# Optimization experiments

Measured on AMD Instinct MI355X. Metric: run time of the kernel, lower is better.

The kernel has to match this reference:

```python
import jax, jax.numpy as jnp
import numpy as np

H = 9
N1, N2, N3 = 100000, 25000, 6250
E1, E2, E3 = 1200000, 300000, 75000
LAYERS = {"l1": (6, 32), "l2": (32, 64), "l3": (64, 128), "l4": (128, 128),
          "r1": (128, 64), "r2": (128, 64), "r3": (64, 32), "r4": (64, 32)}


def setup_inputs() -> dict:
    key = jax.random.key(0)
    ks = iter(jax.random.split(key, 64))
    d = {}
    d["x"] = jax.random.normal(next(ks), (N1, 6), jnp.float32)
    d["ei1"] = jax.random.randint(next(ks), (2, E1), 0, N1)
    d["ei2"] = jax.random.randint(next(ks), (2, E2), 0, N2)
    d["ei3"] = jax.random.randint(next(ks), (2, E3), 0, N3)
    d["clust2"] = jax.random.randint(next(ks), (N1,), 0, N2)
    d["clust3"] = jax.random.randint(next(ks), (N2,), 0, N3)
    for name, (cin, cout) in LAYERS.items():
        d[name + "_u"] = jax.random.normal(next(ks), (cin, H), jnp.float32) * 0.1
        d[name + "_c"] = jax.random.normal(next(ks), (H,), jnp.float32) * 0.1
        d[name + "_w"] = jax.random.normal(next(ks), (cin, H * cout), jnp.float32) * (1.0 / np.sqrt(cin))
        d[name + "_b"] = jnp.zeros((cout,), jnp.float32)
    d["fc1_w"] = jax.random.normal(next(ks), (32, 1024), jnp.float32) * (1.0 / np.sqrt(32))
    d["fc1_b"] = jnp.zeros((1024,), jnp.float32)
    d["fc2_w"] = jax.random.normal(next(ks), (1024, 3), jnp.float32) * (1.0 / np.sqrt(1024))
    d["fc2_b"] = jnp.zeros((3,), jnp.float32)
    return d


def _feast(x, ei, u, c, W, b):
    """FeaStConv (Verma et al., PyG semantics): per-edge head attention
    q = softmax(u^T (x_j - x_i) + c), mean aggregation, self-loops added."""
    n = x.shape[0]
    out = W.shape[1] // H
    loop = jnp.arange(n)
    src = jnp.concatenate([ei[0], loop])  # message source j
    dst = jnp.concatenate([ei[1], loop])  # message target i
    q = jax.nn.softmax((x[src] - x[dst]) @ u + c, axis=1)  # [E, H]
    msg = jnp.zeros((src.shape[0], out), x.dtype)
    for h in range(H):  # fixed head loop keeps peak memory at [E, out]
        msg = msg + q[:, h:h + 1] * (x @ W[:, h * out:(h + 1) * out])[src]
    agg = jax.ops.segment_sum(msg, dst, num_segments=n)
    cnt = jax.ops.segment_sum(jnp.ones((dst.shape[0],), x.dtype), dst, num_segments=n)
    return agg / cnt[:, None] + b  # cnt >= 1 thanks to self-loops


def _pool_mean(x, clust, n_out):
    s = jax.ops.segment_sum(x, clust, num_segments=n_out)
    c = jax.ops.segment_sum(jnp.ones((x.shape[0],), x.dtype), clust, num_segments=n_out)
    return s / jnp.maximum(c, 1.0)[:, None]


def _lrelu(v):
    return jax.nn.leaky_relu(v, 0.1)


def reference(x, ei1, ei2, ei3, clust2, clust3,
              l1_u, l1_c, l1_w, l1_b, l2_u, l2_c, l2_w, l2_b,
              l3_u, l3_c, l3_w, l3_b, l4_u, l4_c, l4_w, l4_b,
              r1_u, r1_c, r1_w, r1_b, r2_u, r2_c, r2_w, r2_b,
              r3_u, r3_c, r3_w, r3_b, r4_u, r4_c, r4_w, r4_b,
              fc1_w, fc1_b, fc2_w, fc2_b):
    x1 = _lrelu(_feast(x, ei1, l1_u, l1_c, l1_w, l1_b))           # [N1, 32]
    x2 = _pool_mean(x1, clust2, N2)                                # [N2, 32]
    x2 = _lrelu(_feast(x2, ei2, l2_u, l2_c, l2_w, l2_b))           # [N2, 64]
    x3 = _pool_mean(x2, clust3, N3)                                # [N3, 64]
    x3 = _lrelu(_feast(x3, ei3, l3_u, l3_c, l3_w, l3_b))           # [N3, 128]
    x3 = _lrelu(_feast(x3, ei3, l4_u, l4_c, l4_w, l4_b))           # [N3, 128]
    f2 = _feast(x3[clust3], ei2, r1_u, r1_c, r1_w, r1_b)           # unpool -> [N2, 64] (no act)
    x2 = jnp.concatenate([x2, f2], axis=1)                         # [N2, 128]
    x2 = _lrelu(_feast(x2, ei2, r2_u, r2_c, r2_w, r2_b))           # [N2, 64]
    f1 = _feast(x2[clust2], ei1, r3_u, r3_c, r3_w, r3_b)           # unpool -> [N1, 32] (no act)
    x1 = jnp.concatenate([x1, f1], axis=1)                         # [N1, 64]
    y = _lrelu(_feast(x1, ei1, r4_u, r4_c, r4_w, r4_b))            # [N1, 32]
    y = _lrelu(y @ fc1_w + fc1_b)                                  # [N1, 1024]
    y = y @ fc2_w + fc2_b                                          # [N1, 3]
    return y / jnp.maximum(jnp.linalg.norm(y, axis=1, keepdims=True), 1e-12)
```

## Files before the change

### kernel.cpp

```cpp
#include <hip/hip_runtime.h>
#include <cstddef>
#include <cstdint>

#define NH 9
#define QLD 16

typedef _Float16 f16x8 __attribute__((ext_vector_type(8)));
typedef _Float16 f16x4 __attribute__((ext_vector_type(4)));
typedef _Float16 f16x2 __attribute__((ext_vector_type(2)));
typedef float f32x4 __attribute__((ext_vector_type(4)));

static const int cN1 = 100000, cN2 = 25000, cN3 = 6250;
static const int cE1 = 1200000, cE2 = 300000, cE3 = 75000;

static inline unsigned ceil_div(size_t a, size_t b) { return (unsigned)((a + b - 1) / b); }

struct PackArgs {
    const float* W[8];
    const float* c[8];
    const float* u[8];
    int K[8], OUT[8], Kpad[8], base[8];
    int total;
};

__global__ void pack_b_all(PackArgs a, _Float16* __restrict__ wt)
{
    int i = blockIdx.x * 256 + threadIdx.x;
    if (i >= a.total) return;
    int li = 0;
#pragma unroll
    for (int j = 1; j < 8; ++j) li += (i >= a.base[j]);
    int r = i - a.base[li];
    int Kp = a.Kpad[li], K = a.K[li], OUT = a.OUT[li];
    int NC = NH * OUT, NCO = NC + OUT;
    int n = r / Kp, k = r % Kp;
    float v = 0.f;
    if (k < K) {
        if (n < NC) v = a.W[li][(size_t)k * NC + n];
        else if (n < NCO) {
            const float* cv = a.c[li];
            float t[NH], m = -1e30f;
#pragma unroll
            for (int h = 0; h < NH; ++h) { t[h] = cv[h]; m = fmaxf(m, t[h]); }
            float den = 0.f;
#pragma unroll
            for (int h = 0; h < NH; ++h) { t[h] = __expf(t[h] - m); den += t[h]; }
            int o = n - NC;
            float acc = 0.f;
#pragma unroll
            for (int h = 0; h < NH; ++h) acc += t[h] * a.W[li][(size_t)k * NC + h * OUT + o];
            v = acc / den;
        } else {
            v = a.u[li][(size_t)k * NH + (n - NCO)];
        }
    }
    wt[i] = (_Float16)v;
}

template <typename AT>
__global__ __launch_bounds__(256) void gemm_merged(
    const AT* __restrict__ A, int lda, const int* __restrict__ ridx,
    const _Float16* __restrict__ WT, int kpad,
    _Float16* __restrict__ C, _Float16* __restrict__ xuh,
    int M, int K, int NC, int OUT)
{
    const int N = NC + OUT + NH;
    const int NCO = NC + OUT;
    const int ldc = NCO + 16;
    const int BM = 64, BK = 32, LK = 40;
    __shared__ _Float16 As[BM][LK];
    __shared__ _Float16 Bs[64][LK];
    const int tid = threadIdx.x;
    const int row0 = blockIdx.y * BM, col0 = blockIdx.x * 64;
    const int lane = tid & 63, wv = tid >> 6;
    const int g = lane >> 4, r16 = lane & 15;
    const int wr = wv >> 1, wc = wv & 1;
    f32x4 acc[2][2] = {};
    for (int k0 = 0; k0 < K; k0 += BK) {
        if constexpr (sizeof(AT) == 2) {
            int r = tid >> 2, c0 = (tid & 3) * 8;
            int gr = row0 + r, gk = k0 + c0;
            f16x8 h = {};
            if (gr < M) {
                int ar = ridx ? ridx[gr] : gr;
                h = *(const f16x8*)((const _Float16*)A + (size_t)ar * lda + gk);
            }
            *(f16x8*)&As[r][c0] = h;
        } else {
            for (int l = tid; l < 512; l += 256) {
                int r = l >> 3, c0 = (l & 7) * 4;
                int gr = row0 + r, gk = k0 + c0;
                float v0 = 0.f, v1 = 0.f, v2 = 0.f, v3 = 0.f;
                if (gr < M) {
                    int ar = ridx ? ridx[gr] : gr;
                    const float* ap = (const float*)A + (size_t)ar * lda + gk;
                    if (gk < K)     v0 = ap[0];
                    if (gk + 1 < K) v1 = ap[1];
                    if (gk + 2 < K) v2 = ap[2];
                    if (gk + 3 < K) v3 = ap[3];
                }
                f16x4 h;
                h[0] = (_Float16)v0; h[1] = (_Float16)v1; h[2] = (_Float16)v2; h[3] = (_Float16)v3;
                *(f16x4*)&As[r][c0] = h;
            }
        }
        {
            int nn = tid >> 2, c0 = (tid & 3) * 8;
            int gn = col0 + nn, gk = k0 + c0;
            f16x8 h = {};
            if (gn < N) h = *(const f16x8*)(WT + (size_t)gn * kpad + gk);
            *(f16x8*)&Bs[nn][c0] = h;
        }
        __syncthreads();
        f16x8 af[2], bf[2];
#pragma unroll
        for (int i = 0; i < 2; ++i) af[i] = *(const f16x8*)&As[wr * 32 + i * 16 + r16][g * 8];
#pragma unroll
        for (int j = 0; j < 2; ++j) bf[j] = *(const f16x8*)&Bs[wc * 32 + j * 16 + r16][g * 8];
#pragma unroll
        for (int i = 0; i < 2; ++i)
#pragma unroll
            for (int j = 0; j < 2; ++j)
                acc[i][j] = __builtin_amdgcn_mfma_f32_16x16x32_f16(af[i], bf[j], acc[i][j], 0, 0, 0);
        __syncthreads();
    }
#pragma unroll
    for (int i = 0; i < 2; ++i)
#pragma unroll
        for (int j = 0; j < 2; ++j) {
            int gc = col0 + wc * 32 + j * 16 + r16;
            if (gc >= N) continue;
            int tcol = gc - NCO;
#pragma unroll
            for (int rr = 0; rr < 4; ++rr) {
                int gr = row0 + wr * 32 + i * 16 + g * 4 + rr;
                if (gr >= M) continue;
                _Float16 val = (_Float16)acc[i][j][rr];
                C[(size_t)gr * ldc + gc] = val;
                if (tcol >= 0) xuh[(size_t)gr * QLD + tcol] = val;
            }
        }
}

__global__ void count_idx(const int* __restrict__ idx, int n, int* __restrict__ cnt)
{
    int i = blockIdx.x * 256 + threadIdx.x;
    if (i < n) atomicAdd(&cnt[idx[i]], 1);
}

__global__ void count_both(const int* __restrict__ src, const int* __restrict__ dst, int E,
                           int* __restrict__ scnt, int* __restrict__ dcnt)
{
    int i = blockIdx.x * 256 + threadIdx.x;
    if (i >= E) return;
    atomicAdd(&scnt[src[i]], 1);
    atomicAdd(&dcnt[dst[i]], 1);
}

__global__ __launch_bounds__(1024) void scan1(const int* __restrict__ in, int* __restrict__ out,
                                              int* __restrict__ part, int n)
{
    __shared__ int wsum[16];
    const int tid = threadIdx.x, lane = tid & 63, wv = tid >> 6;
    int i = blockIdx.x * 1024 + tid;
    int v = (i < n) ? in[i] : 0;
    int acc = v;
#pragma unroll
    for (int off = 1; off < 64; off <<= 1) {
        int t = __shfl_up(acc, off);
        if (lane >= off) acc += t;
    }
    if (lane == 63) wsum[wv] = acc;
    __syncthreads();
    if (wv == 0 && lane < 16) {
        int s = wsum[lane];
        int a2 = s;
#pragma unroll
        for (int off = 1; off < 16; off <<= 1) {
            int t = __shfl_up(a2, off);
            if (lane >= off) a2 += t;
        }
        wsum[lane] = a2 - s;
    }
    __syncthreads();
    int ex = wsum[wv] + acc - v;
    if (i < n) out[i] = ex;
    if (part && tid == 1023) part[blockIdx.x] = ex + v;
}

__global__ void scan_add(int* __restrict__ out, const int* __restrict__ part, int n)
{
    int i = blockIdx.x * 1024 + threadIdx.x;
    if (i < n) out[i] += part[blockIdx.x];
}

__global__ void fill_src(const int* __restrict__ soffB, const int* __restrict__ scnt,
                         int* __restrict__ srcs, int n, int ebias)
{
    int i = blockIdx.x * 256 + threadIdx.x;
    if (i >= n) return;
    int b = soffB[i] - ebias, c = scnt[i];
    for (int k = 0; k < c; ++k) srcs[b + k] = i;
}

__global__ void scatter_light(const int* __restrict__ src, const int* __restrict__ dst, int E,
                              const int* __restrict__ soffB, int* __restrict__ curs,
                              const int* __restrict__ doff, int* __restrict__ curd,
                              int2* __restrict__ erec, int ebias)
{
    int e = blockIdx.x * 256 + threadIdx.x;
    if (e >= E) return;
    int s = src[e], d = dst[e];
    int ps = soffB[s] - ebias + atomicAdd(&curs[s], 1);
    int pd = doff[d] + atomicAdd(&curd[d], 1);
    erec[ps] = make_int2(d, pd);
}

template <int OUT>
__global__ __launch_bounds__(256) void feast_msg(
    const int* __restrict__ srcs, const int2* __restrict__ erec, int E,
    const _Float16* __restrict__ xwa, const _Float16* __restrict__ xuh,
    const float* __restrict__ cvec, _Float16* __restrict__ msg)
{
    constexpr int NC = NH * OUT, NCO = NC + OUT, LDR = NCO + 16;
    const int T = OUT / 16;
    size_t tid = (size_t)blockIdx.x * 256 + threadIdx.x;
    int e = (int)(tid / T);
    int ch = (int)(tid % T);
    if (e >= E) return;
    int s = srcs[e];
    int2 ed = erec[e];
    int d = ed.x, pd = ed.y;
    f16x8 u8s = *(const f16x8*)(xwa + (size_t)s * LDR + NCO);
    f16x2 u2s = *(const f16x2*)(xwa + (size_t)s * LDR + NCO + 8);
    f16x8 u8d = *(const f16x8*)(xuh + (size_t)d * QLD);
    f16x2 u2d = *(const f16x2*)(xuh + (size_t)d * QLD + 8);
    float t[NH];
    float m = -1e30f;
#pragma unroll
    for (int h = 0; h < 8; ++h) {
        t[h] = (float)u8s[h] - (float)u8d[h] + cvec[h];
        m = fmaxf(m, t[h]);
    }
    t[8] = (float)u2s[0] - (float)u2d[0] + cvec[8];
    m = fmaxf(m, t[8]);
    float den = 0.f;
#pragma unroll
    for (int h = 0; h < NH; ++h) { t[h] = __expf(t[h] - m); den += t[h]; }
    float sc = 1.f / den;

    const f16x8* xrow = (const f16x8*)(xwa + (size_t)s * LDR) + ch * 2;
    float acc[16] = {};
#pragma unroll
    for (int h = 0; h < NH; ++h) {
        float qh = t[h] * sc;
        f16x8 a = xrow[h * (OUT / 8)];
        f16x8 b = xrow[h * (OUT / 8) + 1];
#pragma unroll
        for (int j = 0; j < 8; ++j) {
            acc[j]     += qh * (float)a[j];
            acc[8 + j] += qh * (float)b[j];
        }
    }
    f16x8* mo = (f16x8*)(msg + (size_t)pd * OUT + ch * 16);
    f16x8 r0, r1;
#pragma unroll
    for (int j = 0; j < 8; ++j) {
        r0[j] = (_Float16)acc[j];
        r1[j] = (_Float16)acc[8 + j];
    }
    mo[0] = r0;
    mo[1] = r1;
}

template <int OUT>
__global__ __launch_bounds__(256) void feast_red(
    const int* __restrict__ ds,
    const _Float16* __restrict__ msg, const _Float16* __restrict__ xwa,
    const float* __restrict__ bias, _Float16* __restrict__ outp,
    int n, int ldo, int col0, int act,
    const int* __restrict__ clust, float* __restrict__ pooled)
{
    constexpr int NC = NH * OUT, LDR = NC + OUT + 16;
    const int L = OUT / 8;
    size_t tid = (size_t)blockIdx.x * 256 + threadIdx.x;
    int d = (int)(tid / L);
    int p = (int)(tid % L);
    if (d >= n) return;
    int beg = ds[d];
    int end = ds[d + 1];
    int deg = end - beg;
    float acc[8] = {};
    int i = beg;
    for (; i + 4 <= end; i += 4) {
        f16x8 v0 = *(const f16x8*)(msg + (size_t)i * OUT + p * 8);
        f16x8 v1 = *(const f16x8*)(msg + (size_t)(i + 1) * OUT + p * 8);
        f16x8 v2 = *(const f16x8*)(msg + (size_t)(i + 2) * OUT + p * 8);
        f16x8 v3 = *(const f16x8*)(msg + (size_t)(i + 3) * OUT + p * 8);
#pragma unroll
        for (int j = 0; j < 8; ++j)
            acc[j] += ((float)v0[j] + (float)v1[j]) + ((float)v2[j] + (float)v3[j]);
    }
    for (; i < end; ++i) {
        f16x8 v0 = *(const f16x8*)(msg + (size_t)i * OUT + p * 8);
#pragma unroll
        for (int j = 0; j < 8; ++j) acc[j] += (float)v0[j];
    }
    float sc = 1.f / (float)(deg + 1);
    f16x8 sv = *(const f16x8*)(xwa + (size_t)d * LDR + NC + p * 8);
    float o[8];
    f16x8 oh;
#pragma unroll
    for (int j = 0; j < 8; ++j) {
        float v = (acc[j] + (float)sv[j]) * sc + bias[p * 8 + j];
        if (act) v = v > 0.f ? v : 0.1f * v;
        o[j] = v;
        oh[j] = (_Float16)v;
    }
    *(f16x8*)(outp + (size_t)d * ldo + col0 + p * 8) = oh;
    if (clust) {
        float* pp = pooled + (size_t)clust[d] * OUT + p * 8;
#pragma unroll
        for (int j = 0; j < 8; ++j) unsafeAtomicAdd(&pp[j], o[j]);
    }
}

__global__ void pool_div(float* __restrict__ pooled, const int* __restrict__ pcnt, int C, int m)
{
    size_t tid = (size_t)blockIdx.x * 256 + threadIdx.x;
    int j = (int)(tid / C);
    if (j >= m) return;
    pooled[tid] /= fmaxf((float)pcnt[j], 1.f);
}

__global__ void w1_to_f16t(const float* __restrict__ w1, _Float16* __restrict__ w1t)
{
    int i = blockIdx.x * 256 + threadIdx.x;
    if (i >= 32 * 1024) return;
    int n = i >> 5, k = i & 31;
    w1t[i] = (_Float16)w1[k * 1024 + n];
}

__global__ __launch_bounds__(256) void fc_head2(
    const _Float16* __restrict__ yin, const _Float16* __restrict__ w1t,
    const float* __restrict__ b1, const float* __restrict__ w2,
    const float* __restrict__ b2, float* __restrict__ outp, int n)
{
    const int lane = threadIdx.x & 63, wv = threadIdx.x >> 6;
    const int g = lane >> 4, r16 = lane & 15;
    const int node0 = blockIdx.x * 64 + wv * 16;

    f16x8 afrag = {};
    int anode = node0 + r16;
    if (anode < n) afrag = *(const f16x8*)(yin + (size_t)anode * 32 + g * 8);

    float o0[4] = {0.f, 0.f, 0.f, 0.f};
    float o1[4] = {0.f, 0.f, 0.f, 0.f};
    float o2[4] = {0.f, 0.f, 0.f, 0.f};
    const f32x4 zero4 = {0.f, 0.f, 0.f, 0.f};

#pragma unroll 2
    for (int t = 0; t < 64; ++t) {
        const f16x8 bfrag = *(const f16x8*)(w1t + ((size_t)(t * 16 + r16)) * 32 + g * 8);
        f32x4 d = __builtin_amdgcn_mfma_f32_16x16x32_f16(afrag, bfrag, zero4, 0, 0, 0);
        int kh = t * 16 + r16;
        float b1v = b1[kh];
        float w20 = w2[kh * 3], w21 = w2[kh * 3 + 1], w22 = w2[kh * 3 + 2];
#pragma unroll
        for (int r = 0; r < 4; ++r) {
            float h = d[r] + b1v;
            h = h > 0.f ? h : 0.1f * h;
            o0[r] += h * w20;
            o1[r] += h * w21;
            o2[r] += h * w22;
        }
    }
#pragma unroll
    for (int r = 0; r < 4; ++r) {
#pragma unroll
        for (int off = 1; off < 16; off <<= 1) {
            o0[r] += __shfl_xor(o0[r], off);
            o1[r] += __shfl_xor(o1[r], off);
            o2[r] += __shfl_xor(o2[r], off);
        }
    }
    if (r16 == 0) {
#pragma unroll
        for (int r = 0; r < 4; ++r) {
            int node = node0 + g * 4 + r;
            if (node >= n) continue;
            float v0 = o0[r] + b2[0];
            float v1 = o1[r] + b2[1];
            float v2 = o2[r] + b2[2];
            float nr = fmaxf(sqrtf(v0 * v0 + v1 * v1 + v2 * v2), 1e-12f);
            outp[(size_t)node * 3 + 0] = v0 / nr;
            outp[(size_t)node * 3 + 1] = v1 / nr;
            outp[(size_t)node * 3 + 2] = v2 / nr;
        }
    }
}

static void launch_msg(int outC, const int* srcs, const int2* erec, int E,
                       const _Float16* xwa, const _Float16* xuh, const float* cvec,
                       _Float16* msg, hipStream_t stream)
{
    dim3 g(ceil_div((size_t)E * (outC / 16), 256));
    if (outC == 32)       feast_msg<32><<<g, 256, 0, stream>>>(srcs, erec, E, xwa, xuh, cvec, msg);
    else if (outC == 64)  feast_msg<64><<<g, 256, 0, stream>>>(srcs, erec, E, xwa, xuh, cvec, msg);
    else                  feast_msg<128><<<g, 256, 0, stream>>>(srcs, erec, E, xwa, xuh, cvec, msg);
}

static void launch_red(int outC, const int* ds,
                       const _Float16* msg, const _Float16* xwa, const float* bias,
                       _Float16* outp, int n, int ldo, int col0, int act,
                       const int* clust, float* pooled, hipStream_t stream)
{
    dim3 g(ceil_div((size_t)n * (outC / 8), 256));
    if (outC == 32)       feast_red<32><<<g, 256, 0, stream>>>(ds, msg, xwa, bias, outp, n, ldo, col0, act, clust, pooled);
    else if (outC == 64)  feast_red<64><<<g, 256, 0, stream>>>(ds, msg, xwa, bias, outp, n, ldo, col0, act, clust, pooled);
    else                  feast_red<128><<<g, 256, 0, stream>>>(ds, msg, xwa, bias, outp, n, ldo, col0, act, clust, pooled);
}

extern "C" void kernel_launch(void* const* d_in, const int* in_sizes, int n_in,
                              void* d_out, int out_size, void* d_ws, size_t ws_size,
                              hipStream_t stream)
{
    const float* x      = (const float*)d_in[0];
    const int*   ei1    = (const int*)d_in[1];
    const int*   ei2    = (const int*)d_in[2];
    const int*   ei3    = (const int*)d_in[3];
    const int*   clust2 = (const int*)d_in[4];
    const int*   clust3 = (const int*)d_in[5];
    const float* lp[8][4];
    for (int i = 0; i < 8; ++i)
        for (int j = 0; j < 4; ++j)
            lp[i][j] = (const float*)d_in[6 + i * 4 + j];
    const float* fc1_w = (const float*)d_in[38];
    const float* fc1_b = (const float*)d_in[39];
    const float* fc2_w = (const float*)d_in[40];
    const float* fc2_b = (const float*)d_in[41];
    float* out = (float*)d_out;

    static const int lK[8]   = {6, 32, 64, 128, 128, 128, 64, 64};
    static const int lOUT[8] = {32, 64, 128, 128, 64, 64, 32, 32};

    char* ws = (char*)d_ws;
    size_t off = 0;
    auto alloc = [&](size_t b) { size_t p = off; off += (b + 255) & ~(size_t)255; return p; };
    _Float16* XWA = (_Float16*)(ws + alloc((size_t)cN1 * 336 * 2));
    _Float16* MSG = (_Float16*)(ws + alloc((size_t)cE1 * 32 * 2));
    _Float16* XUH = (_Float16*)(ws + alloc((size_t)cN1 * QLD * 2));
    _Float16* X1CAT = (_Float16*)(ws + alloc((size_t)cN1 * 64 * 2));
    _Float16* X2CAT = (_Float16*)(ws + alloc((size_t)cN2 * 128 * 2));
    _Float16* X2B   = (_Float16*)(ws + alloc((size_t)cN2 * 64 * 2));
    _Float16* X3    = (_Float16*)(ws + alloc((size_t)cN3 * 128 * 2));
    _Float16* YB    = (_Float16*)(ws + alloc((size_t)cN1 * 32 * 2));
    float* GATH = (float*)(ws + alloc((size_t)cN2 * 32 * 4));
    float* P3   = (float*)(ws + alloc((size_t)cN3 * 64 * 4));
    int* SRCS1 = (int*)(ws + alloc((size_t)cE1 * 4));
    int* SRCS2 = (int*)(ws + alloc((size_t)cE2 * 4));
    int* SRCS3 = (int*)(ws + alloc((size_t)cE3 * 4));
    int2* EREC1 = (int2*)(ws + alloc((size_t)cE1 * 8));
    int2* EREC2 = (int2*)(ws + alloc((size_t)cE2 * 8));
    int2* EREC3 = (int2*)(ws + alloc((size_t)cE3 * 8));
    int* DS1 = (int*)(ws + alloc((size_t)2 * cN1 * 4));
    int* DS2 = (int*)(ws + alloc((size_t)2 * cN2 * 4));
    int* DS3 = (int*)(ws + alloc((size_t)2 * cN3 * 4));
    size_t zn = (size_t)4 * (cN1 + cN2 + cN3) + cN2 + cN3;
    int* ZBLK = (int*)(ws + alloc(zn * 4));
    int* CB1 = ZBLK;
    int* CURS1 = CB1 + 2 * cN1;
    int* CURD1 = CURS1 + cN1;
    int* CB2 = CURD1 + cN1;
    int* CURS2 = CB2 + 2 * cN2;
    int* CURD2 = CURS2 + cN2;
    int* CB3 = CURD2 + cN2;
    int* CURS3 = CB3 + 2 * cN3;
    int* CURD3 = CURS3 + cN3;
    int* PC2 = CURD3 + cN3;
    int* PC3 = PC2 + cN2;
    int* PART = (int*)(ws + alloc(1024 * 4));
    _Float16* W1T = (_Float16*)(ws + alloc((size_t)32 * 1024 * 2));
    PackArgs pa;
    int ptot = 0;
    for (int i = 0; i < 8; ++i) {
        pa.W[i] = lp[i][2]; pa.c[i] = lp[i][1]; pa.u[i] = lp[i][0];
        pa.K[i] = lK[i]; pa.OUT[i] = lOUT[i];
        pa.Kpad[i] = (lK[i] + 31) & ~31;
        pa.base[i] = ptot;
        ptot += (NH * lOUT[i] + lOUT[i] + NH) * pa.Kpad[i];
    }
    pa.total = ptot;
    _Float16* WT = (_Float16*)(ws + alloc((size_t)ptot * 2));

    auto run_scan = [&](const int* in, int* outp, int n) {
        int nb = (n + 1023) / 1024;
        scan1<<<nb, 1024, 0, stream>>>(in, outp, nb > 1 ? PART : nullptr, n);
        if (nb > 1) {
            scan1<<<1, 1024, 0, stream>>>(PART, PART, nullptr, nb);
            scan_add<<<nb, 1024, 0, stream>>>(outp, PART, n);
        }
    };

    hipMemsetAsync(ZBLK, 0, zn * 4, stream);

    auto build = [&](const int* ei, int E, int n, int* cb, int* curs, int* curd, int* ds,
                     int* srcs, int2* erec) {
        count_both<<<ceil_div(E, 256), 256, 0, stream>>>(ei, ei + E, E, cb + n, cb);
        run_scan(cb, ds, 2 * n);
        fill_src<<<ceil_div(n, 256), 256, 0, stream>>>(ds + n, cb + n, srcs, n, E);
        scatter_light<<<ceil_div(E, 256), 256, 0, stream>>>(ei, ei + E, E, ds + n, curs, ds, curd, erec, E);
    };
    build(ei1, cE1, cN1, CB1, CURS1, CURD1, DS1, SRCS1, EREC1);
    build(ei2, cE2, cN2, CB2, CURS2, CURD2, DS2, SRCS2, EREC2);
    build(ei3, cE3, cN3, CB3, CURS3, CURD3, DS3, SRCS3, EREC3);

    pack_b_all<<<ceil_div(ptot, 256), 256, 0, stream>>>(pa, WT);
    w1_to_f16t<<<ceil_div(32 * 1024, 256), 256, 0, stream>>>(fc1_w, W1T);

    auto feast = [&](auto* xin, int ldx, const int* ridx, int n, int cin, int li,
                     const int* srcs, const int2* erec, const int* ds, int E,
                     _Float16* dstp, int ldo, int col0, int act,
                     const int* pclust, float* pooled) {
        int outC = lOUT[li];
        int NC = NH * outC;
        int N = NC + outC + NH;
        gemm_merged<<<dim3(ceil_div(N, 64), ceil_div(n, 64)), 256, 0, stream>>>(
            xin, ldx, ridx, WT + (size_t)pa.base[li], pa.Kpad[li], XWA, XUH, n, cin, NC, outC);
        launch_msg(outC, srcs, erec, E, XWA, XUH, lp[li][1], MSG, stream);
        launch_red(outC, ds, MSG, XWA, lp[li][3], dstp, n, ldo, col0, act, pclust, pooled, stream);
    };

    hipMemsetAsync(GATH, 0, (size_t)cN2 * 32 * 4, stream);
    count_idx<<<ceil_div(cN1, 256), 256, 0, stream>>>(clust2, cN1, PC2);
    feast(x, 6, nullptr, cN1, 6, 0, SRCS1, EREC1, DS1, cE1, X1CAT, 64, 0, 1, clust2, GATH);
    pool_div<<<ceil_div((size_t)cN2 * 32, 256), 256, 0, stream>>>(GATH, PC2, 32, cN2);

    count_idx<<<ceil_div(cN2, 256), 256, 0, stream>>>(clust3, cN2, PC3);
    hipMemsetAsync(P3, 0, (size_t)cN3 * 64 * 4, stream);
    feast(GATH, 32, nullptr, cN2, 32, 1, SRCS2, EREC2, DS2, cE2, X2CAT, 128, 0, 1, clust3, P3);
    pool_div<<<ceil_div((size_t)cN3 * 64, 256), 256, 0, stream>>>(P3, PC3, 64, cN3);

    feast(P3, 64, nullptr, cN3, 64, 2, SRCS3, EREC3, DS3, cE3, X3, 128, 0, 1, nullptr, nullptr);
    feast(X3, 128, nullptr, cN3, 128, 3, SRCS3, EREC3, DS3, cE3, X3, 128, 0, 1, nullptr, nullptr);

    feast(X3, 128, clust3, cN2, 128, 4, SRCS2, EREC2, DS2, cE2, X2CAT, 128, 64, 0, nullptr, nullptr);

    feast(X2CAT, 128, nullptr, cN2, 128, 5, SRCS2, EREC2, DS2, cE2, X2B, 64, 0, 1, nullptr, nullptr);

    feast(X2B, 64, clust2, cN1, 64, 6, SRCS1, EREC1, DS1, cE1, X1CAT, 64, 32, 0, nullptr, nullptr);

    feast(X1CAT, 64, nullptr, cN1, 64, 7, SRCS1, EREC1, DS1, cE1, YB, 32, 0, 1, nullptr, nullptr);

    fc_head2<<<ceil_div(cN1, 64), 256, 0, stream>>>(YB, W1T, fc1_b, fc2_w, fc2_b, out, cN1);

    (void)in_sizes; (void)n_in; (void)out_size; (void)ws_size;
}
```

Before: 991.3 us.

## Two-pass coarse binning of edges by source before CSR scatter

```diff
diff --git a/kernel.cpp b/kernel.cpp
--- a/kernel.cpp
+++ b/kernel.cpp
@@ -148,13 +148,16 @@
     if (i < n) atomicAdd(&cnt[idx[i]], 1);
 }
 
-__global__ void count_both(const int* __restrict__ src, const int* __restrict__ dst, int E,
-                           int* __restrict__ scnt, int* __restrict__ dcnt)
+__global__ void count_b3(const int* __restrict__ src, const int* __restrict__ dst, int E,
+                         int* __restrict__ scnt, int* __restrict__ dcnt,
+                         int* __restrict__ bcnt, int shift)
 {
     int i = blockIdx.x * 256 + threadIdx.x;
     if (i >= E) return;
-    atomicAdd(&scnt[src[i]], 1);
+    int s = src[i];
+    atomicAdd(&scnt[s], 1);
     atomicAdd(&dcnt[dst[i]], 1);
+    atomicAdd(&bcnt[s >> shift], 1);
 }
 
 __global__ __launch_bounds__(1024) void scan1(const int* __restrict__ in, int* __restrict__ out,
@@ -203,14 +206,27 @@
     for (int k = 0; k < c; ++k) srcs[b + k] = i;
 }
 
-__global__ void scatter_light(const int* __restrict__ src, const int* __restrict__ dst, int E,
-                              const int* __restrict__ soffB, int* __restrict__ curs,
-                              const int* __restrict__ doff, int* __restrict__ curd,
-                              int2* __restrict__ erec, int ebias)
+__global__ void bin_pass1(const int* __restrict__ src, const int* __restrict__ dst, int E,
+                          const int* __restrict__ boff, int* __restrict__ bcur,
+                          int2* __restrict__ tmp, int shift)
 {
     int e = blockIdx.x * 256 + threadIdx.x;
     if (e >= E) return;
-    int s = src[e], d = dst[e];
+    int s = src[e];
+    int b = s >> shift;
+    int p = boff[b] + atomicAdd(&bcur[b], 1);
+    tmp[p] = make_int2(s, dst[e]);
+}
+
+__global__ void bin_pass2(const int2* __restrict__ tmp, int E,
+                          const int* __restrict__ soffB, int* __restrict__ curs,
+                          const int* __restrict__ doff, int* __restrict__ curd,
+                          int2* __restrict__ erec, int ebias)
+{
+    int e = blockIdx.x * 256 + threadIdx.x;
+    if (e >= E) return;
+    int2 rec = tmp[e];
+    int s = rec.x, d = rec.y;
     int ps = soffB[s] - ebias + atomicAdd(&curs[s], 1);
     int pd = doff[d] + atomicAdd(&curd[d], 1);
     erec[ps] = make_int2(d, pd);
@@ -443,6 +459,10 @@
 
     static const int lK[8]   = {6, 32, 64, 128, 128, 128, 64, 64};
     static const int lOUT[8] = {32, 64, 128, 128, 64, 64, 32, 32};
+    static const int lSH[3]  = {5, 3, 1};
+    const int NB1 = ceil_div(cN1, 1 << lSH[0]);
+    const int NB2 = ceil_div(cN2, 1 << lSH[1]);
+    const int NB3 = ceil_div(cN3, 1 << lSH[2]);
 
     char* ws = (char*)d_ws;
     size_t off = 0;
@@ -463,21 +483,29 @@
     int2* EREC1 = (int2*)(ws + alloc((size_t)cE1 * 8));
     int2* EREC2 = (int2*)(ws + alloc((size_t)cE2 * 8));
     int2* EREC3 = (int2*)(ws + alloc((size_t)cE3 * 8));
+    int2* TMP = (int2*)(ws + alloc((size_t)cE1 * 8));
     int* DS1 = (int*)(ws + alloc((size_t)2 * cN1 * 4));
     int* DS2 = (int*)(ws + alloc((size_t)2 * cN2 * 4));
     int* DS3 = (int*)(ws + alloc((size_t)2 * cN3 * 4));
-    size_t zn = (size_t)4 * (cN1 + cN2 + cN3) + cN2 + cN3;
+    int* BOFF = (int*)(ws + alloc((size_t)4096 * 4));
+    size_t zn = (size_t)4 * (cN1 + cN2 + cN3) + 2 * (NB1 + NB2 + NB3) + cN2 + cN3;
     int* ZBLK = (int*)(ws + alloc(zn * 4));
     int* CB1 = ZBLK;
     int* CURS1 = CB1 + 2 * cN1;
     int* CURD1 = CURS1 + cN1;
-    int* CB2 = CURD1 + cN1;
+    int* BCNT1 = CURD1 + cN1;
+    int* BCUR1 = BCNT1 + NB1;
+    int* CB2 = BCUR1 + NB1;
     int* CURS2 = CB2 + 2 * cN2;
     int* CURD2 = CURS2 + cN2;
-    int* CB3 = CURD2 + cN2;
+    int* BCNT2 = CURD2 + cN2;
+    int* BCUR2 = BCNT2 + NB2;
+    int* CB3 = BCUR2 + NB2;
     int* CURS3 = CB3 + 2 * cN3;
     int* CURD3 = CURS3 + cN3;
-    int* PC2 = CURD3 + cN3;
+    int* BCNT3 = CURD3 + cN3;
+    int* BCUR3 = BCNT3 + NB3;
+    int* PC2 = BCUR3 + NB3;
     int* PC3 = PC2 + cN2;
     int* PART = (int*)(ws + alloc(1024 * 4));
     _Float16* W1T = (_Float16*)(ws + alloc((size_t)32 * 1024 * 2));
@@ -504,16 +532,19 @@
 
     hipMemsetAsync(ZBLK, 0, zn * 4, stream);
 
-    auto build = [&](const int* ei, int E, int n, int* cb, int* curs, int* curd, int* ds,
+    auto build = [&](const int* ei, int E, int n, int* cb, int* curs, int* curd,
+                     int* bcnt, int* bcur, int nb, int shift, int* ds,
                      int* srcs, int2* erec) {
-        count_both<<<ceil_div(E, 256), 256, 0, stream>>>(ei, ei + E, E, cb + n, cb);
+        count_b3<<<ceil_div(E, 256), 256, 0, stream>>>(ei, ei + E, E, cb + n, cb, bcnt, shift);
         run_scan(cb, ds, 2 * n);
+        run_scan(bcnt, BOFF, nb);
         fill_src<<<ceil_div(n, 256), 256, 0, stream>>>(ds + n, cb + n, srcs, n, E);
-        scatter_light<<<ceil_div(E, 256), 256, 0, stream>>>(ei, ei + E, E, ds + n, curs, ds, curd, erec, E);
+        bin_pass1<<<ceil_div(E, 256), 256, 0, stream>>>(ei, ei + E, E, BOFF, bcur, TMP, shift);
+        bin_pass2<<<ceil_div(E, 256), 256, 0, stream>>>(TMP, E, ds + n, curs, ds, curd, erec, E);
     };
-    build(ei1, cE1, cN1, CB1, CURS1, CURD1, DS1, SRCS1, EREC1);
-    build(ei2, cE2, cN2, CB2, CURS2, CURD2, DS2, SRCS2, EREC2);
-    build(ei3, cE3, cN3, CB3, CURS3, CURD3, DS3, SRCS3, EREC3);
+    build(ei1, cE1, cN1, CB1, CURS1, CURD1, BCNT1, BCUR1, NB1, lSH[0], DS1, SRCS1, EREC1);
+    build(ei2, cE2, cN2, CB2, CURS2, CURD2, BCNT2, BCUR2, NB2, lSH[1], DS2, SRCS2, EREC2);
+    build(ei3, cE3, cN3, CB3, CURS3, CURD3, BCNT3, BCUR3, NB3, lSH[2], DS3, SRCS3, EREC3);
 
     pack_b_all<<<ceil_div(ptot, 256), 256, 0, stream>>>(pa, WT);
     w1_to_f16t<<<ceil_div(32 * 1024, 256), 256, 0, stream>>>(fc1_w, W1T);
```

Result: slower. 1.258 ms (+26.9%).
